# Kernel optimization log

Measured on AMD Instinct MI355X. Metric: run time of the kernel, lower is better.

The kernel has to match this reference:

```python
import jax, jax.numpy as jnp
import numpy as np

SPS_AMPLIFY = 1.5
SPS_DAMPEN = 0.3
SPS_DEEP_QUESTION = 0.1
SPS_EXCLAIM = 0.85
SPS_QUESTION = 0.25
SPS_SUPER_EXCLAIM = 0.95

B, S, D = 4, 2048, 1024
NUM_HEADS = 16
HEAD_DIM = D // NUM_HEADS
SCALE = HEAD_DIM ** (-0.5)


def sps_pro(x):
    """Piecewise elementwise modulation based on sigmoid(x) bands."""
    xn = jax.nn.sigmoid(x)
    # bands: xn>0.95 -> 2.0 ; 0.85<xn<=0.95 -> 1.5 ; xn<0.1 -> 0.1 ;
    #        0.1<=xn<0.25 -> 0.3 ; else -> 1.0
    mult = jnp.where(
        xn > SPS_SUPER_EXCLAIM, 2.0,
        jnp.where(xn > SPS_EXCLAIM, SPS_AMPLIFY,
                  jnp.where(xn < SPS_DEEP_QUESTION, 0.1,
                            jnp.where(xn < SPS_QUESTION, SPS_DAMPEN, 1.0))))
    return x * mult


def setup_inputs() -> dict:
    key = jax.random.key(0)
    k0, k1, k2, k3, k4 = jax.random.split(key, 5)
    s = 1.0 / np.sqrt(D)
    return {
        "x": jax.random.normal(k0, (B, S, D), dtype=jnp.float32),
        "W_qkv": jax.random.uniform(k1, (D, 3 * D), dtype=jnp.float32, minval=-s, maxval=s),
        "b_qkv": jax.random.uniform(k2, (3 * D,), dtype=jnp.float32, minval=-s, maxval=s),
        "W_proj": jax.random.uniform(k3, (D, D), dtype=jnp.float32, minval=-s, maxval=s),
        "b_proj": jax.random.uniform(k4, (D,), dtype=jnp.float32, minval=-s, maxval=s),
    }


def reference(x, W_qkv, b_qkv, W_proj, b_proj):
    qkv = jnp.einsum('bsd,de->bse', x, W_qkv) + b_qkv  # [B,S,3D]
    q, k, v = jnp.split(qkv, 3, axis=-1)               # each [B,S,D]
    attn = jnp.einsum('bsd,btd->bst', q, k) * SCALE    # [B,S,S]
    attn = sps_pro(attn)
    attn = jax.nn.softmax(attn, axis=-1)
    out = jnp.einsum('bst,btd->bsd', attn, v)          # [B,S,D]
    out = jnp.einsum('bsd,de->bse', out, W_proj) + b_proj
    return out
```

## Files before the change

kernel.cpp:

```cpp
#include <hip/hip_runtime.h>
#include <hip/hip_bf16.h>
#include <hip/hip_fp16.h>
#include <stdint.h>

typedef __attribute__((ext_vector_type(8))) _Float16 f16x8;
typedef __attribute__((ext_vector_type(4))) float f32x4;

__device__ __forceinline__ void async16(void* lds, const void* g) {
  __builtin_amdgcn_global_load_lds(
      (const __attribute__((address_space(1))) void*)g,
      (__attribute__((address_space(3))) void*)lds, 16, 0, 0);
}

__device__ __forceinline__ uint16_t f2h_u(float f) {
  union { __half h; uint16_t u; } c;
  c.h = __float2half(f);
  return c.u;
}

__global__ __launch_bounds__(256)
void conv_f2h(const float* __restrict__ in, uint16_t* __restrict__ out, int n4) {
  int i = blockIdx.x * 256 + threadIdx.x;
  if (i >= n4) return;
  float4 v = ((const float4*)in)[i];
  ushort4 o;
  o.x = f2h_u(v.x); o.y = f2h_u(v.y); o.z = f2h_u(v.z); o.w = f2h_u(v.w);
  ((ushort4*)out)[i] = o;
}

__global__ __launch_bounds__(256)
void trans_f2h(const float* __restrict__ in, uint16_t* __restrict__ out,
               int ldin, int ldout) {
  __shared__ float t[64][65];
  const int tx = threadIdx.x & 63, ty = threadIdx.x >> 6;
  const int r0 = blockIdx.y * 64, c0 = blockIdx.x * 64;
#pragma unroll
  for (int i = 0; i < 16; ++i)
    t[ty + i * 4][tx] = in[(size_t)(r0 + ty + i * 4) * ldin + c0 + tx];
  __syncthreads();
#pragma unroll
  for (int i = 0; i < 16; ++i)
    out[(size_t)(c0 + ty + i * 4) * ldout + r0 + tx] = f2h_u(t[tx][ty + i * 4]);
}

template <int EPI>
__global__ __launch_bounds__(512, 2)
void gemm8p(const uint16_t* __restrict__ A, const uint16_t* __restrict__ B,
            void* __restrict__ Cv, void* __restrict__ Cv2, void* __restrict__ Cv3,
            const float* __restrict__ bias,
            int nT, int lda, int ldb, int ldc,
            long long strA, long long strB, long long strC) {
  extern __shared__ uint16_t lds_u16[];

  const int gx = gridDim.x, gy = gridDim.y;
  const int nwg = gx * gy * gridDim.z;
  const int fid = blockIdx.x + gx * (blockIdx.y + gy * blockIdx.z);
  const int fs = (fid & 7) * (nwg >> 3) + (fid >> 3);
  const int bx = fs % gx;
  const int by = (fs / gx) % gy;
  const int bz = fs / (gx * gy);

  const int tid = threadIdx.x;
  const int l = tid & 63;
  const int w = tid >> 6;
  const int wm = w >> 2, wn = w & 3;
  const int l15 = l & 15, l4 = l >> 4;
  const int rowBase = bx * 256, colBase = by * 256;
  const uint16_t* Ag = A + (size_t)bz * strA;
  const uint16_t* Bg = B + (size_t)bz * strB;

  const uint16_t* sA[2][2];
  const uint16_t* sB[2][2];
#pragma unroll
  for (int u = 0; u < 2; ++u) {
    int c = tid + (u << 9);
    int cs = c ^ ((c >> 3) & 7);
    int row = cs >> 3, kc = (cs & 7) * 8;
    sA[0][u] = Ag + (size_t)(rowBase + row) * lda + kc;
    sA[1][u] = Ag + (size_t)(rowBase + 128 + row) * lda + kc;
    sB[0][u] = Bg + (size_t)(colBase + row) * ldb + kc;
    sB[1][u] = Bg + (size_t)(colBase + 128 + row) * ldb + kc;
  }

  f32x4 acc[8][4];
#pragma unroll
  for (int m = 0; m < 8; ++m)
#pragma unroll
    for (int n = 0; n < 4; ++n)
      acc[m][n] = (f32x4){0.f, 0.f, 0.f, 0.f};

#define SH_A(buf, h, koff)                                                     \
  {                                                                            \
    const uint32_t d_ = (buf)*32768u + (h)*8192u;                              \
    async16(&lds_u16[d_ + (size_t)tid * 8], sA[h][0] + (koff));                \
    async16(&lds_u16[d_ + (size_t)(tid + 512) * 8], sA[h][1] + (koff));        \
  }
#define SH_B(buf, h, koff)                                                     \
  {                                                                            \
    const uint32_t d_ = (buf)*32768u + 16384u + (h)*8192u;                     \
    async16(&lds_u16[d_ + (size_t)tid * 8], sB[h][0] + (koff));                \
    async16(&lds_u16[d_ + (size_t)(tid + 512) * 8], sB[h][1] + (koff));        \
  }
#define RD_A(dst, buf, mh)                                                     \
  _Pragma("unroll") for (int mr = 0; mr < 4; ++mr) {                           \
    const int lr = (mh)*64 + mr * 16 + l15;                                    \
    const char* hb = (const char*)lds_u16 + (buf)*65536 + wm * 16384;          \
    _Pragma("unroll") for (int ks = 0; ks < 2; ++ks)                           \
      dst[mr][ks] = *(const f16x8*)(hb + lr * 128 +                            \
                    ((ks * 64 + l4 * 16) ^ ((lr & 7) << 4)));                  \
  }
#define RD_B(dst, buf, nh)                                                     \
  _Pragma("unroll") for (int nr = 0; nr < 2; ++nr) {                           \
    const int lr = (wn & 1) * 64 + (nh)*32 + nr * 16 + l15;                    \
    const char* hb = (const char*)lds_u16 + (buf)*65536 + 32768 +              \
                     (wn >> 1) * 16384;                                        \
    _Pragma("unroll") for (int ks = 0; ks < 2; ++ks)                           \
      dst[nr][ks] = *(const f16x8*)(hb + lr * 128 +                            \
                    ((ks * 64 + l4 * 16) ^ ((lr & 7) << 4)));                  \
  }
#define MM(m0, n0, AF, BF)                                                     \
  __builtin_amdgcn_s_setprio(1);                                               \
  _Pragma("unroll") for (int ks = 0; ks < 2; ++ks)                             \
  _Pragma("unroll") for (int mr = 0; mr < 4; ++mr)                             \
  _Pragma("unroll") for (int nr = 0; nr < 2; ++nr)                             \
    acc[(m0) + mr][(n0) + nr] = __builtin_amdgcn_mfma_f32_16x16x32_f16(        \
        AF[mr][ks], BF[nr][ks], acc[(m0) + mr][(n0) + nr], 0, 0, 0);           \
  __builtin_amdgcn_s_setprio(0);
#define VMC(n) asm volatile("s_waitcnt vmcnt(" #n ")" ::: "memory");
#define BAR() __builtin_amdgcn_s_barrier();

  SH_A(0, 0, 0) SH_A(0, 1, 0) SH_B(0, 0, 0) SH_B(0, 1, 0)
  SH_B(1, 0, 64) SH_B(1, 1, 64)
  VMC(4)
  BAR()

  const int nIter = nT >> 1;
  for (int i = 0; i < nIter; ++i) {
    const int e2 = 2 * i + 2, o = 2 * i + 1, o2 = 2 * i + 3;
    const int ke2 = e2 << 6, ko = o << 6, ko2 = o2 << 6;
    f16x8 a0[4][2], a1[4][2], b0[2][2], b1[2][2];
    RD_A(a0, 0, 0) RD_B(b0, 0, 0)
    SH_A(1, 0, ko)
    BAR()
    MM(0, 0, a0, b0)
    RD_B(b1, 0, 1)
    SH_A(1, 1, ko)
    BAR()
    MM(0, 2, a0, b1)
    RD_A(a1, 0, 1)
    if (e2 < nT) SH_B(0, 0, ke2)
    BAR()
    MM(4, 2, a1, b1)
    if (e2 < nT) { SH_B(0, 1, ke2) VMC(4) } else { VMC(0) }
    BAR()
    MM(4, 0, a1, b0)
    RD_A(a0, 1, 0) RD_B(b0, 1, 0)
    if (e2 < nT) SH_A(0, 0, ke2)
    BAR()
    MM(0, 0, a0, b0)
    RD_B(b1, 1, 1)
    if (e2 < nT) SH_A(0, 1, ke2)
    BAR()
    MM(0, 2, a0, b1)
    RD_A(a1, 1, 1)
    if (o2 < nT) SH_B(1, 0, ko2)
    BAR()
    MM(4, 2, a1, b1)
    if (o2 < nT) { SH_B(1, 1, ko2) }
    if (i + 1 < nIter) { if (o2 < nT) { VMC(4) } else { VMC(0) } }
    BAR()
    MM(4, 0, a1, b0)
  }
#undef SH_A
#undef SH_B
#undef RD_A
#undef RD_B
#undef MM
#undef VMC
#undef BAR

  if (EPI == 0) {
    uint16_t* qd = (uint16_t*)Cv;
    uint16_t* kd = (uint16_t*)Cv2;
    uint16_t* vt = (uint16_t*)Cv3;
#pragma unroll
    for (int ni = 0; ni < 4; ++ni) {
      const int gcol = colBase + wn * 64 + ni * 16 + l15;
      const float bv = bias[gcol];
      if (gcol < 2048) {
        uint16_t* base = (gcol < 1024 ? qd : kd) + (gcol & 1023);
#pragma unroll
        for (int mi = 0; mi < 8; ++mi)
#pragma unroll
          for (int j = 0; j < 4; ++j) {
            const int grow = rowBase + wm * 128 + mi * 16 + l4 * 4 + j;
            base[(size_t)(grow >> 11) * 2097152 + (size_t)(grow & 2047) * 1024] =
                f2h_u(acc[mi][ni][j] + bv);
          }
      } else {
        const int d = gcol - 2048;
#pragma unroll
        for (int mi = 0; mi < 8; ++mi) {
          const int grow0 = rowBase + wm * 128 + mi * 16 + l4 * 4;
          ushort4 o;
          o.x = f2h_u(acc[mi][ni][0] + bv);
          o.y = f2h_u(acc[mi][ni][1] + bv);
          o.z = f2h_u(acc[mi][ni][2] + bv);
          o.w = f2h_u(acc[mi][ni][3] + bv);
          *(ushort4*)&vt[(size_t)(grow0 >> 11) * 2097152 + (size_t)d * 2048 +
                         (grow0 & 2047)] = o;
        }
      }
    }
  }
}

template <int EPI>
__global__ __launch_bounds__(256, 2)
void gemm_mb(const uint16_t* __restrict__ A, const uint16_t* __restrict__ B,
             void* __restrict__ Cv, const float* __restrict__ bias,
             float* __restrict__ rowsum,
             int nT, int lda, int ldb, int ldc,
             long long strA, long long strB, long long strC) {
  extern __shared__ uint16_t lds_u16[];

  const int gx = gridDim.x, gy = gridDim.y;
  const int nwg = gx * gy * gridDim.z;
  const int fid = blockIdx.x + gx * (blockIdx.y + gy * blockIdx.z);
  const int fs = (fid & 7) * (nwg >> 3) + (fid >> 3);
  const int bx = fs % gx;
  const int by = (fs / gx) % gy;
  const int bz = fs / (gx * gy);

  const int tid = threadIdx.x;
  const int l = tid & 63;
  const int w = tid >> 6;
  const int wm = w >> 1, wn = w & 1;
  const int l15 = l & 15, l4 = l >> 4;
  const int rowBase = bx * 128, colBase = by * 128;
  const uint16_t* Ag = A + (size_t)bz * strA;
  const uint16_t* Bg = B + (size_t)bz * strB;

  const uint16_t* pA[4];
  const uint16_t* pB[4];
#pragma unroll
  for (int u = 0; u < 4; ++u) {
    int c = tid + (u << 8);
    int cs = c ^ ((c >> 3) & 7);
    pA[u] = Ag + (size_t)(rowBase + (cs >> 3)) * lda + (cs & 7) * 8;
    pB[u] = Bg + (size_t)(colBase + (cs >> 3)) * ldb + (cs & 7) * 8;
  }

  f32x4 acc[4][4];
#pragma unroll
  for (int m = 0; m < 4; ++m)
#pragma unroll
    for (int n = 0; n < 4; ++n)
      acc[m][n] = (f32x4){0.f, 0.f, 0.f, 0.f};

#define STAGE(t2, s2)                                                          \
  {                                                                            \
    const int kb_ = (t2) << 6;                                                 \
    uint16_t* dA_ = lds_u16 + (s2)*16384;                                      \
    uint16_t* dB_ = dA_ + 8192;                                                \
    _Pragma("unroll") for (int u = 0; u < 4; ++u) {                            \
      async16(&dA_[(size_t)(tid + (u << 8)) * 8], pA[u] + kb_);                \
      async16(&dB_[(size_t)(tid + (u << 8)) * 8], pB[u] + kb_);                \
    }                                                                          \
  }

  STAGE(0, 0)
  asm volatile("s_waitcnt vmcnt(0)" ::: "memory");
  __builtin_amdgcn_s_barrier();

  for (int t = 0; t < nT; ++t) {
    const int s = t & 1;
    if (t + 1 < nT) STAGE(t + 1, s ^ 1)
    const uint16_t* As = lds_u16 + s * 16384;
    const uint16_t* Bs = As + 8192;
#pragma unroll
    for (int ks = 0; ks < 2; ++ks) {
      f16x8 af[4], bf[4];
#pragma unroll
      for (int m = 0; m < 4; ++m) {
        const int r = wm * 64 + m * 16 + l15;
        const int byt = r * 128 + ((ks * 64 + l4 * 16) ^ ((r & 7) << 4));
        af[m] = *(const f16x8*)((const char*)As + byt);
      }
#pragma unroll
      for (int n = 0; n < 4; ++n) {
        const int r = wn * 64 + n * 16 + l15;
        const int byt = r * 128 + ((ks * 64 + l4 * 16) ^ ((r & 7) << 4));
        bf[n] = *(const f16x8*)((const char*)Bs + byt);
      }
      __builtin_amdgcn_s_setprio(1);
#pragma unroll
      for (int m = 0; m < 4; ++m)
#pragma unroll
        for (int n = 0; n < 4; ++n)
          acc[m][n] = __builtin_amdgcn_mfma_f32_16x16x32_f16(af[m], bf[n], acc[m][n], 0, 0, 0);
      __builtin_amdgcn_s_setprio(0);
    }
    if (t + 1 < nT) {
      asm volatile("s_waitcnt vmcnt(0)" ::: "memory");
      __builtin_amdgcn_s_barrier();
    }
  }
#undef STAGE

  const int orow0 = rowBase + wm * 64 + l4 * 4;
  const int ocol0 = colBase + wn * 64 + l15;
  if (EPI == 5) {
    uint16_t* C = (uint16_t*)Cv + (size_t)bz * strC;
    float* rs_b = rowsum + (size_t)bz * 2048;
#pragma unroll
    for (int m = 0; m < 4; ++m)
#pragma unroll
      for (int j = 0; j < 4; ++j) {
        const int grow = orow0 + m * 16 + j;
        float rs = 0.f;
#pragma unroll
        for (int n = 0; n < 4; ++n) {
          float xs = acc[m][n][j] * 0.125f;
          float mult = (xs > 2.94443897916644f) ? 2.0f
                     : (xs > 1.73460105538811f) ? 1.5f
                     : (xs < -2.19722457733622f) ? 0.1f
                     : (xs < -1.09861228866811f) ? 0.3f
                                                 : 1.0f;
          float e = __expf(fminf(xs * mult, 19.0f) - 8.0f);
          C[(size_t)grow * ldc + ocol0 + n * 16] = f2h_u(e);
          rs += e;
        }
        rs += __shfl_xor(rs, 1);
        rs += __shfl_xor(rs, 2);
        rs += __shfl_xor(rs, 4);
        rs += __shfl_xor(rs, 8);
        if (l15 == 0) atomicAdd(&rs_b[grow], rs);
      }
  } else if (EPI == 6) {
    uint16_t* C = (uint16_t*)Cv + (size_t)bz * strC;
    const float* rs_b = rowsum + (size_t)bz * 2048;
#pragma unroll
    for (int m = 0; m < 4; ++m)
#pragma unroll
      for (int j = 0; j < 4; ++j) {
        const int grow = orow0 + m * 16 + j;
        const float inv = 1.0f / rs_b[grow];
#pragma unroll
        for (int n = 0; n < 4; ++n)
          C[(size_t)grow * ldc + ocol0 + n * 16] = f2h_u(acc[m][n][j] * inv);
      }
  } else {
    float* C = (float*)Cv;
#pragma unroll
    for (int n = 0; n < 4; ++n) {
      const float bv = bias[ocol0 + n * 16];
#pragma unroll
      for (int m = 0; m < 4; ++m)
#pragma unroll
        for (int j = 0; j < 4; ++j)
          C[(size_t)(orow0 + m * 16 + j) * ldc + ocol0 + n * 16] = acc[m][n][j] + bv;
    }
  }
}

extern "C" void kernel_launch(void* const* d_in, const int* in_sizes, int n_in,
                              void* d_out, int out_size, void* d_ws, size_t ws_size,
                              hipStream_t stream) {
  const float* x     = (const float*)d_in[0];
  const float* Wqkv  = (const float*)d_in[1];
  const float* bqkv  = (const float*)d_in[2];
  const float* Wproj = (const float*)d_in[3];
  const float* bproj = (const float*)d_in[4];
  float* out = (float*)d_out;

  char* ws = (char*)d_ws;
  size_t off = 0;
  auto alloc = [&](size_t bytes) -> void* {
    void* p = ws + off;
    off += (bytes + 255) & ~(size_t)255;
    return p;
  };
  uint16_t* xh     = (uint16_t*)alloc(8192ULL * 1024 * 2);
  uint16_t* WqkvT  = (uint16_t*)alloc(3072ULL * 1024 * 2);
  uint16_t* WpT    = (uint16_t*)alloc(1024ULL * 1024 * 2);
  uint16_t* qh     = (uint16_t*)alloc(4ULL * 2048 * 1024 * 2);
  uint16_t* kh     = (uint16_t*)alloc(4ULL * 2048 * 1024 * 2);
  uint16_t* vT     = (uint16_t*)alloc(4ULL * 1024 * 2048 * 2);
  uint16_t* Pm     = (uint16_t*)alloc(4ULL * 2048 * 2048 * 2);
  float*    rowsum = (float*)alloc(4ULL * 2048 * 4);
  uint16_t* ao     = xh;

  hipMemsetAsync(rowsum, 0, 4ULL * 2048 * 4, stream);
  conv_f2h<<<8192, 256, 0, stream>>>(x, xh, 2097152);
  trans_f2h<<<dim3(48, 16), 256, 0, stream>>>(Wqkv, WqkvT, 3072, 1024);
  trans_f2h<<<dim3(16, 16), 256, 0, stream>>>(Wproj, WpT, 1024, 1024);
  gemm8p<0><<<dim3(32, 12, 1), 512, 131072, stream>>>(
      xh, WqkvT, qh, kh, vT, bqkv, 16, 1024, 1024, 0, 0, 0, 0);
  gemm_mb<5><<<dim3(16, 16, 4), 256, 65536, stream>>>(
      qh, kh, Pm, nullptr, rowsum, 16, 1024, 1024, 2048,
      2097152LL, 2097152LL, 4194304LL);
  gemm_mb<6><<<dim3(16, 8, 4), 256, 65536, stream>>>(
      Pm, vT, ao, nullptr, rowsum, 32, 2048, 2048, 1024,
      4194304LL, 2097152LL, 2097152LL);
  gemm_mb<4><<<dim3(64, 8, 1), 256, 65536, stream>>>(
      ao, WpT, out, bproj, nullptr, 16, 1024, 1024, 1024, 0, 0, 0);
}
```

Measured before the change: 213.9 us.

## Switch attention GEMMs to 4-stage K=32 pipeline and replace rowsum atomics with partials

The three batched GEMMs move from a double-buffered K=64 loop to a four-stage ring of K=32 tiles in the same LDS budget. Loads are issued three tiles ahead with graded vmcnt waits, and a new 2-bit XOR swizzle matches the 64-byte rows. The softmax row-sum atomics and their memset are replaced by per-tile partial sums written to a buffer, then reduced by a small extra kernel. The deeper pipeline is meant to hide more global latency, at the cost of twice as many barriers and smaller MFMA batches per barrier.

```diff
diff --git a/kernel.cpp b/kernel.cpp
--- a/kernel.cpp
+++ b/kernel.cpp
@@ -41,6 +41,20 @@
 #pragma unroll
   for (int i = 0; i < 16; ++i)
     out[(size_t)(c0 + ty + i * 4) * ldout + r0 + tx] = f2h_u(t[tx][ty + i * 4]);
+}
+
+__global__ __launch_bounds__(256)
+void reduce_part(const float* __restrict__ part, float* __restrict__ rowsum, int n) {
+  int i = blockIdx.x * 256 + threadIdx.x;
+  if (i >= n) return;
+  const float4* p = (const float4*)(part + (size_t)i * 32);
+  float s = 0.f;
+#pragma unroll
+  for (int q = 0; q < 8; ++q) {
+    float4 v = p[q];
+    s += (v.x + v.y) + (v.z + v.w);
+  }
+  rowsum[i] = s;
 }
 
 template <int EPI>
@@ -217,9 +231,9 @@
 
 template <int EPI>
 __global__ __launch_bounds__(256, 2)
-void gemm_mb(const uint16_t* __restrict__ A, const uint16_t* __restrict__ B,
+void gemm_r4(const uint16_t* __restrict__ A, const uint16_t* __restrict__ B,
              void* __restrict__ Cv, const float* __restrict__ bias,
-             float* __restrict__ rowsum,
+             float* __restrict__ raux,
              int nT, int lda, int ldb, int ldc,
              long long strA, long long strB, long long strC) {
   extern __shared__ uint16_t lds_u16[];
@@ -237,18 +251,20 @@
   const int w = tid >> 6;
   const int wm = w >> 1, wn = w & 1;
   const int l15 = l & 15, l4 = l >> 4;
+  const int gl = (l15 ^ (l15 >> 2)) & 3;
   const int rowBase = bx * 128, colBase = by * 128;
   const uint16_t* Ag = A + (size_t)bz * strA;
   const uint16_t* Bg = B + (size_t)bz * strB;
 
-  const uint16_t* pA[4];
-  const uint16_t* pB[4];
-#pragma unroll
-  for (int u = 0; u < 4; ++u) {
+  const uint16_t* pA[2];
+  const uint16_t* pB[2];
+#pragma unroll
+  for (int u = 0; u < 2; ++u) {
     int c = tid + (u << 8);
-    int cs = c ^ ((c >> 3) & 7);
-    pA[u] = Ag + (size_t)(rowBase + (cs >> 3)) * lda + (cs & 7) * 8;
-    pB[u] = Bg + (size_t)(colBase + (cs >> 3)) * ldb + (cs & 7) * 8;
+    int r = c >> 2, s = c & 3;
+    int kc = (s ^ ((r ^ (r >> 2)) & 3)) * 8;
+    pA[u] = Ag + (size_t)(rowBase + r) * lda + kc;
+    pB[u] = Bg + (size_t)(colBase + r) * ldb + kc;
   }
 
   f32x4 acc[4][4];
@@ -258,61 +274,65 @@
     for (int n = 0; n < 4; ++n)
       acc[m][n] = (f32x4){0.f, 0.f, 0.f, 0.f};
 
-#define STAGE(t2, s2)                                                          \
+#define STAGE(t2)                                                              \
   {                                                                            \
-    const int kb_ = (t2) << 6;                                                 \
-    uint16_t* dA_ = lds_u16 + (s2)*16384;                                      \
-    uint16_t* dB_ = dA_ + 8192;                                                \
-    _Pragma("unroll") for (int u = 0; u < 4; ++u) {                            \
+    const int kb_ = (t2) << 5;                                                 \
+    uint16_t* dA_ = lds_u16 + ((t2) & 3) * 8192;                               \
+    uint16_t* dB_ = dA_ + 4096;                                                \
+    _Pragma("unroll") for (int u = 0; u < 2; ++u) {                            \
       async16(&dA_[(size_t)(tid + (u << 8)) * 8], pA[u] + kb_);                \
       async16(&dB_[(size_t)(tid + (u << 8)) * 8], pB[u] + kb_);                \
     }                                                                          \
   }
-
-  STAGE(0, 0)
-  asm volatile("s_waitcnt vmcnt(0)" ::: "memory");
+#define VMC(n) asm volatile("s_waitcnt vmcnt(" #n ")" ::: "memory");
+
+  STAGE(0)
+  STAGE(1)
+  STAGE(2)
+  VMC(8)
   __builtin_amdgcn_s_barrier();
 
   for (int t = 0; t < nT; ++t) {
-    const int s = t & 1;
-    if (t + 1 < nT) STAGE(t + 1, s ^ 1)
-    const uint16_t* As = lds_u16 + s * 16384;
-    const uint16_t* Bs = As + 8192;
-#pragma unroll
-    for (int ks = 0; ks < 2; ++ks) {
-      f16x8 af[4], bf[4];
-#pragma unroll
-      for (int m = 0; m < 4; ++m) {
-        const int r = wm * 64 + m * 16 + l15;
-        const int byt = r * 128 + ((ks * 64 + l4 * 16) ^ ((r & 7) << 4));
-        af[m] = *(const f16x8*)((const char*)As + byt);
+    if (t + 3 < nT) STAGE(t + 3)
+    const char* As = (const char*)(lds_u16 + (t & 3) * 8192);
+    const char* Bs = As + 8192;
+    f16x8 af[4], bf[4];
+#pragma unroll
+    for (int m = 0; m < 4; ++m) {
+      const int r = wm * 64 + m * 16 + l15;
+      af[m] = *(const f16x8*)(As + r * 64 + ((l4 ^ gl) << 4));
+    }
+#pragma unroll
+    for (int n = 0; n < 4; ++n) {
+      const int r = wn * 64 + n * 16 + l15;
+      bf[n] = *(const f16x8*)(Bs + r * 64 + ((l4 ^ gl) << 4));
+    }
+    __builtin_amdgcn_s_setprio(1);
+#pragma unroll
+    for (int m = 0; m < 4; ++m)
+#pragma unroll
+      for (int n = 0; n < 4; ++n)
+        acc[m][n] = __builtin_amdgcn_mfma_f32_16x16x32_f16(af[m], bf[n], acc[m][n], 0, 0, 0);
+    __builtin_amdgcn_s_setprio(0);
+    if (t + 1 < nT) {
+      if (t + 3 < nT) {
+        VMC(8)
+      } else if (t + 2 < nT) {
+        VMC(4)
+      } else {
+        VMC(0)
       }
-#pragma unroll
-      for (int n = 0; n < 4; ++n) {
-        const int r = wn * 64 + n * 16 + l15;
-        const int byt = r * 128 + ((ks * 64 + l4 * 16) ^ ((r & 7) << 4));
-        bf[n] = *(const f16x8*)((const char*)Bs + byt);
-      }
-      __builtin_amdgcn_s_setprio(1);
-#pragma unroll
-      for (int m = 0; m < 4; ++m)
-#pragma unroll
-        for (int n = 0; n < 4; ++n)
-          acc[m][n] = __builtin_amdgcn_mfma_f32_16x16x32_f16(af[m], bf[n], acc[m][n], 0, 0, 0);
-      __builtin_amdgcn_s_setprio(0);
-    }
-    if (t + 1 < nT) {
-      asm volatile("s_waitcnt vmcnt(0)" ::: "memory");
       __builtin_amdgcn_s_barrier();
     }
   }
 #undef STAGE
+#undef VMC
 
   const int orow0 = rowBase + wm * 64 + l4 * 4;
   const int ocol0 = colBase + wn * 64 + l15;
   if (EPI == 5) {
     uint16_t* C = (uint16_t*)Cv + (size_t)bz * strC;
-    float* rs_b = rowsum + (size_t)bz * 2048;
+    float* part = raux;
 #pragma unroll
     for (int m = 0; m < 4; ++m)
 #pragma unroll
@@ -335,11 +355,12 @@
         rs += __shfl_xor(rs, 2);
         rs += __shfl_xor(rs, 4);
         rs += __shfl_xor(rs, 8);
-        if (l15 == 0) atomicAdd(&rs_b[grow], rs);
+        if (l15 == 0)
+          part[((size_t)bz * 2048 + grow) * 32 + by * 2 + wn] = rs;
       }
   } else if (EPI == 6) {
     uint16_t* C = (uint16_t*)Cv + (size_t)bz * strC;
-    const float* rs_b = rowsum + (size_t)bz * 2048;
+    const float* rs_b = raux + (size_t)bz * 2048;
 #pragma unroll
     for (int m = 0; m < 4; ++m)
 #pragma unroll
@@ -388,21 +409,22 @@
   uint16_t* kh     = (uint16_t*)alloc(4ULL * 2048 * 1024 * 2);
   uint16_t* vT     = (uint16_t*)alloc(4ULL * 1024 * 2048 * 2);
   uint16_t* Pm     = (uint16_t*)alloc(4ULL * 2048 * 2048 * 2);
+  float*    part   = (float*)alloc(4ULL * 2048 * 32 * 4);
   float*    rowsum = (float*)alloc(4ULL * 2048 * 4);
   uint16_t* ao     = xh;
 
-  hipMemsetAsync(rowsum, 0, 4ULL * 2048 * 4, stream);
   conv_f2h<<<8192, 256, 0, stream>>>(x, xh, 2097152);
   trans_f2h<<<dim3(48, 16), 256, 0, stream>>>(Wqkv, WqkvT, 3072, 1024);
   trans_f2h<<<dim3(16, 16), 256, 0, stream>>>(Wproj, WpT, 1024, 1024);
   gemm8p<0><<<dim3(32, 12, 1), 512, 131072, stream>>>(
       xh, WqkvT, qh, kh, vT, bqkv, 16, 1024, 1024, 0, 0, 0, 0);
-  gemm_mb<5><<<dim3(16, 16, 4), 256, 65536, stream>>>(
-      qh, kh, Pm, nullptr, rowsum, 16, 1024, 1024, 2048,
+  gemm_r4<5><<<dim3(16, 16, 4), 256, 65536, stream>>>(
+      qh, kh, Pm, nullptr, part, 32, 1024, 1024, 2048,
       2097152LL, 2097152LL, 4194304LL);
-  gemm_mb<6><<<dim3(16, 8, 4), 256, 65536, stream>>>(
-      Pm, vT, ao, nullptr, rowsum, 32, 2048, 2048, 1024,
+  reduce_part<<<32, 256, 0, stream>>>(part, rowsum, 8192);
+  gemm_r4<6><<<dim3(16, 8, 4), 256, 65536, stream>>>(
+      Pm, vT, ao, nullptr, rowsum, 64, 2048, 2048, 1024,
       4194304LL, 2097152LL, 2097152LL);
-  gemm_mb<4><<<dim3(64, 8, 1), 256, 65536, stream>>>(
-      ao, WpT, out, bproj, nullptr, 16, 1024, 1024, 1024, 0, 0, 0);
-}
+  gemm_r4<4><<<dim3(64, 8, 1), 256, 65536, stream>>>(
+      ao, WpT, out, bproj, nullptr, 32, 1024, 1024, 1024, 0, 0, 0);
+}
```

Result: slower. 228.2 us (+6.7%).

## Fold output projection into V weights to remove final projection GEMM

Applied to the files above, without the earlier changes.

Uses associativity: P·(xWv + bv)·Wp = P·(x·(Wv·Wp) + bv·Wp). A small 1024×1024 GEMM precomputes Wv·Wp (transposed, fp16) into the V slice of the QKV weights, and a small kernel computes bv·Wp as the new V bias. The PV GEMM then writes normalized fp32 output plus b_proj directly, so the separate 8192×1024×1024 projection GEMM disappears. The cost is an extra weight-side GEMM per call, plus the extra rounding of the fused weight product to fp16.

```diff
diff --git a/kernel.cpp b/kernel.cpp
--- a/kernel.cpp
+++ b/kernel.cpp
@@ -29,6 +29,16 @@
 }
 
 __global__ __launch_bounds__(256)
+void conv_wv(const float* __restrict__ in, uint16_t* __restrict__ out) {
+  int i = blockIdx.x * 256 + threadIdx.x;
+  int r = i >> 8, c4 = (i & 255) * 4;
+  float4 v = *(const float4*)&in[(size_t)r * 3072 + 2048 + c4];
+  ushort4 o;
+  o.x = f2h_u(v.x); o.y = f2h_u(v.y); o.z = f2h_u(v.z); o.w = f2h_u(v.w);
+  *(ushort4*)&out[(size_t)r * 1024 + c4] = o;
+}
+
+__global__ __launch_bounds__(256)
 void trans_f2h(const float* __restrict__ in, uint16_t* __restrict__ out,
                int ldin, int ldout) {
   __shared__ float t[64][65];
@@ -43,11 +53,20 @@
     out[(size_t)(c0 + ty + i * 4) * ldout + r0 + tx] = f2h_u(t[tx][ty + i * 4]);
 }
 
+__global__ __launch_bounds__(256)
+void bvp_kernel(const float* __restrict__ bv, const float* __restrict__ Wproj,
+                float* __restrict__ bvp) {
+  int j = blockIdx.x * 256 + threadIdx.x;
+  float s = 0.f;
+  for (int k = 0; k < 1024; ++k) s = fmaf(bv[k], Wproj[(size_t)k * 1024 + j], s);
+  bvp[j] = s;
+}
+
 template <int EPI>
 __global__ __launch_bounds__(512, 2)
 void gemm8p(const uint16_t* __restrict__ A, const uint16_t* __restrict__ B,
             void* __restrict__ Cv, void* __restrict__ Cv2, void* __restrict__ Cv3,
-            const float* __restrict__ bias,
+            const float* __restrict__ bias, const float* __restrict__ bias2,
             int nT, int lda, int ldb, int ldc,
             long long strA, long long strB, long long strC) {
   extern __shared__ uint16_t lds_u16[];
@@ -186,8 +205,8 @@
 #pragma unroll
     for (int ni = 0; ni < 4; ++ni) {
       const int gcol = colBase + wn * 64 + ni * 16 + l15;
-      const float bv = bias[gcol];
       if (gcol < 2048) {
+        const float bv = bias[gcol];
         uint16_t* base = (gcol < 1024 ? qd : kd) + (gcol & 1023);
 #pragma unroll
         for (int mi = 0; mi < 8; ++mi)
@@ -199,6 +218,7 @@
           }
       } else {
         const int d = gcol - 2048;
+        const float bv = bias2[d];
 #pragma unroll
         for (int mi = 0; mi < 8; ++mi) {
           const int grow0 = rowBase + wm * 128 + mi * 16 + l4 * 4;
@@ -337,8 +357,8 @@
         rs += __shfl_xor(rs, 8);
         if (l15 == 0) atomicAdd(&rs_b[grow], rs);
       }
-  } else if (EPI == 6) {
-    uint16_t* C = (uint16_t*)Cv + (size_t)bz * strC;
+  } else if (EPI == 7) {
+    float* C = (float*)Cv + (size_t)bz * strC;
     const float* rs_b = rowsum + (size_t)bz * 2048;
 #pragma unroll
     for (int m = 0; m < 4; ++m)
@@ -348,19 +368,18 @@
         const float inv = 1.0f / rs_b[grow];
 #pragma unroll
         for (int n = 0; n < 4; ++n)
-          C[(size_t)grow * ldc + ocol0 + n * 16] = f2h_u(acc[m][n][j] * inv);
+          C[(size_t)grow * ldc + ocol0 + n * 16] =
+              acc[m][n][j] * inv + bias[ocol0 + n * 16];
       }
   } else {
-    float* C = (float*)Cv;
-#pragma unroll
-    for (int n = 0; n < 4; ++n) {
-      const float bv = bias[ocol0 + n * 16];
+    uint16_t* C = (uint16_t*)Cv + (size_t)bz * strC;
+#pragma unroll
+    for (int n = 0; n < 4; ++n)
 #pragma unroll
       for (int m = 0; m < 4; ++m)
 #pragma unroll
         for (int j = 0; j < 4; ++j)
-          C[(size_t)(orow0 + m * 16 + j) * ldc + ocol0 + n * 16] = acc[m][n][j] + bv;
-    }
+          C[(size_t)(orow0 + m * 16 + j) * ldc + ocol0 + n * 16] = f2h_u(acc[m][n][j]);
   }
 }
 
@@ -384,25 +403,29 @@
   uint16_t* xh     = (uint16_t*)alloc(8192ULL * 1024 * 2);
   uint16_t* WqkvT  = (uint16_t*)alloc(3072ULL * 1024 * 2);
   uint16_t* WpT    = (uint16_t*)alloc(1024ULL * 1024 * 2);
+  uint16_t* Wvh    = (uint16_t*)alloc(1024ULL * 1024 * 2);
   uint16_t* qh     = (uint16_t*)alloc(4ULL * 2048 * 1024 * 2);
   uint16_t* kh     = (uint16_t*)alloc(4ULL * 2048 * 1024 * 2);
   uint16_t* vT     = (uint16_t*)alloc(4ULL * 1024 * 2048 * 2);
   uint16_t* Pm     = (uint16_t*)alloc(4ULL * 2048 * 2048 * 2);
   float*    rowsum = (float*)alloc(4ULL * 2048 * 4);
-  uint16_t* ao     = xh;
+  float*    bvp    = (float*)alloc(1024ULL * 4);
 
   hipMemsetAsync(rowsum, 0, 4ULL * 2048 * 4, stream);
   conv_f2h<<<8192, 256, 0, stream>>>(x, xh, 2097152);
-  trans_f2h<<<dim3(48, 16), 256, 0, stream>>>(Wqkv, WqkvT, 3072, 1024);
+  conv_wv<<<1024, 256, 0, stream>>>(Wqkv, Wvh);
+  trans_f2h<<<dim3(32, 16), 256, 0, stream>>>(Wqkv, WqkvT, 3072, 1024);
   trans_f2h<<<dim3(16, 16), 256, 0, stream>>>(Wproj, WpT, 1024, 1024);
+  gemm_mb<3><<<dim3(8, 8, 1), 256, 65536, stream>>>(
+      WpT, Wvh, WqkvT + 2048ULL * 1024, nullptr, nullptr,
+      16, 1024, 1024, 1024, 0, 0, 0);
+  bvp_kernel<<<4, 256, 0, stream>>>(bqkv + 2048, Wproj, bvp);
   gemm8p<0><<<dim3(32, 12, 1), 512, 131072, stream>>>(
-      xh, WqkvT, qh, kh, vT, bqkv, 16, 1024, 1024, 0, 0, 0, 0);
+      xh, WqkvT, qh, kh, vT, bqkv, bvp, 16, 1024, 1024, 0, 0, 0, 0);
   gemm_mb<5><<<dim3(16, 16, 4), 256, 65536, stream>>>(
       qh, kh, Pm, nullptr, rowsum, 16, 1024, 1024, 2048,
       2097152LL, 2097152LL, 4194304LL);
-  gemm_mb<6><<<dim3(16, 8, 4), 256, 65536, stream>>>(
-      Pm, vT, ao, nullptr, rowsum, 32, 2048, 2048, 1024,
+  gemm_mb<7><<<dim3(16, 8, 4), 256, 65536, stream>>>(
+      Pm, vT, out, bproj, rowsum, 32, 2048, 2048, 1024,
       4194304LL, 2097152LL, 2097152LL);
-  gemm_mb<4><<<dim3(64, 8, 1), 256, 65536, stream>>>(
-      ao, WpT, out, bproj, nullptr, 16, 1024, 1024, 1024, 0, 0, 0);
-}
+}
```

New measurement: 234.7 us. 9.7% more time.

## Compute V transposed via separate swapped-operand GEMM instead of strided epilogue stores

Applied to the files above, without the earlier changes.

The fused QKV GEMM now produces only Q and K. V^T is computed by a separate gemm_mb launch with swapped operands (W_v^T times x), so its outputs land in transposed layout and are stored contiguously along the sequence dimension. Previously the V columns were written with strided 8-byte scattered stores from the big GEMM epilogue. The cost is an extra kernel launch and a smaller first GEMM grid, which may lower utilization.

```diff
diff --git a/kernel.cpp b/kernel.cpp
--- a/kernel.cpp
+++ b/kernel.cpp
@@ -46,7 +46,7 @@
 template <int EPI>
 __global__ __launch_bounds__(512, 2)
 void gemm8p(const uint16_t* __restrict__ A, const uint16_t* __restrict__ B,
-            void* __restrict__ Cv, void* __restrict__ Cv2, void* __restrict__ Cv3,
+            void* __restrict__ Cv, void* __restrict__ Cv2,
             const float* __restrict__ bias,
             int nT, int lda, int ldb, int ldc,
             long long strA, long long strB, long long strC) {
@@ -182,35 +182,19 @@
   if (EPI == 0) {
     uint16_t* qd = (uint16_t*)Cv;
     uint16_t* kd = (uint16_t*)Cv2;
-    uint16_t* vt = (uint16_t*)Cv3;
 #pragma unroll
     for (int ni = 0; ni < 4; ++ni) {
       const int gcol = colBase + wn * 64 + ni * 16 + l15;
       const float bv = bias[gcol];
-      if (gcol < 2048) {
-        uint16_t* base = (gcol < 1024 ? qd : kd) + (gcol & 1023);
-#pragma unroll
-        for (int mi = 0; mi < 8; ++mi)
-#pragma unroll
-          for (int j = 0; j < 4; ++j) {
-            const int grow = rowBase + wm * 128 + mi * 16 + l4 * 4 + j;
-            base[(size_t)(grow >> 11) * 2097152 + (size_t)(grow & 2047) * 1024] =
-                f2h_u(acc[mi][ni][j] + bv);
-          }
-      } else {
-        const int d = gcol - 2048;
-#pragma unroll
-        for (int mi = 0; mi < 8; ++mi) {
-          const int grow0 = rowBase + wm * 128 + mi * 16 + l4 * 4;
-          ushort4 o;
-          o.x = f2h_u(acc[mi][ni][0] + bv);
-          o.y = f2h_u(acc[mi][ni][1] + bv);
-          o.z = f2h_u(acc[mi][ni][2] + bv);
-          o.w = f2h_u(acc[mi][ni][3] + bv);
-          *(ushort4*)&vt[(size_t)(grow0 >> 11) * 2097152 + (size_t)d * 2048 +
-                         (grow0 & 2047)] = o;
+      uint16_t* base = (gcol < 1024 ? qd : kd) + (gcol & 1023);
+#pragma unroll
+      for (int mi = 0; mi < 8; ++mi)
+#pragma unroll
+        for (int j = 0; j < 4; ++j) {
+          const int grow = rowBase + wm * 128 + mi * 16 + l4 * 4 + j;
+          base[(size_t)(grow >> 11) * 2097152 + (size_t)(grow & 2047) * 1024] =
+              f2h_u(acc[mi][ni][j] + bv);
         }
-      }
     }
   }
 }
@@ -310,7 +294,19 @@
 
   const int orow0 = rowBase + wm * 64 + l4 * 4;
   const int ocol0 = colBase + wn * 64 + l15;
-  if (EPI == 5) {
+  if (EPI == 2) {
+    uint16_t* C = (uint16_t*)Cv + (size_t)bz * strC;
+#pragma unroll
+    for (int m = 0; m < 4; ++m)
+#pragma unroll
+      for (int j = 0; j < 4; ++j) {
+        const int d = orow0 + m * 16 + j;
+        const float bv = bias[d];
+#pragma unroll
+        for (int n = 0; n < 4; ++n)
+          C[(size_t)d * ldc + ocol0 + n * 16] = f2h_u(acc[m][n][j] + bv);
+      }
+  } else if (EPI == 5) {
     uint16_t* C = (uint16_t*)Cv + (size_t)bz * strC;
     float* rs_b = rowsum + (size_t)bz * 2048;
 #pragma unroll
@@ -395,8 +391,11 @@
   conv_f2h<<<8192, 256, 0, stream>>>(x, xh, 2097152);
   trans_f2h<<<dim3(48, 16), 256, 0, stream>>>(Wqkv, WqkvT, 3072, 1024);
   trans_f2h<<<dim3(16, 16), 256, 0, stream>>>(Wproj, WpT, 1024, 1024);
-  gemm8p<0><<<dim3(32, 12, 1), 512, 131072, stream>>>(
-      xh, WqkvT, qh, kh, vT, bqkv, 16, 1024, 1024, 0, 0, 0, 0);
+  gemm8p<0><<<dim3(32, 8, 1), 512, 131072, stream>>>(
+      xh, WqkvT, qh, kh, bqkv, 16, 1024, 1024, 0, 0, 0, 0);
+  gemm_mb<2><<<dim3(8, 16, 4), 256, 65536, stream>>>(
+      WqkvT + 2048ULL * 1024, xh, vT, bqkv + 2048, nullptr,
+      16, 1024, 1024, 2048, 0, 2097152LL, 2097152LL);
   gemm_mb<5><<<dim3(16, 16, 4), 256, 65536, stream>>>(
       qh, kh, Pm, nullptr, rowsum, 16, 1024, 1024, 2048,
       2097152LL, 2097152LL, 4194304LL);
```

Measured after the change: 207.0 us. 3.2% less time.
